# Kernel optimization log

Hardware: AMD Instinct MI355X
Metric: run time of the kernel (lower is better)

The kernel has to match this reference:

```python
import jax, jax.numpy as jnp
import numpy as np

N_ENT = 4096
N_REL = 4
F = 128
BATCH = 8192
ADJ_DENSITY = 0.01


def setup_inputs() -> dict:
    key = jax.random.key(0)
    ks = jax.random.split(key, 8)
    features = jax.random.normal(ks[0], (N_ENT, F), dtype=jnp.float32)
    # sparse binary adjacency per relation (matches count_nonzero degree normalization)
    adj = (jax.random.uniform(ks[1], (N_REL, N_ENT, N_ENT)) < ADJ_DENSITY).astype(jnp.float32)
    W1 = jax.random.normal(ks[2], (N_REL, F, F), dtype=jnp.float32)  # [R, out, in]
    W2 = jax.random.normal(ks[3], (N_REL, F, F), dtype=jnp.float32)
    # DistMult init: diagonal relation matrices (full params, as in the torch code)
    diag_vals = jax.random.normal(ks[4], (N_REL, F), dtype=jnp.float32)
    relmats = jax.vmap(jnp.diag)(diag_vals)  # [R, F, F]
    e1_idx = jax.random.randint(ks[5], (BATCH,), 0, N_ENT)
    rel_idx = jax.random.randint(ks[6], (BATCH,), 0, N_REL)
    e2_idx = jax.random.randint(ks[7], (BATCH,), 0, N_ENT)
    return {"features": features, "adj": adj, "W1": W1, "W2": W2,
            "relmats": relmats, "e1_idx": e1_idx, "rel_idx": rel_idx, "e2_idx": e2_idx}


def _conv_layer(adj, feat, W):
    # degree normalization: 1 / count_nonzero(A_r, dim=1), zeros -> 1
    deg = jnp.sum(adj != 0, axis=2).astype(feat.dtype)            # [R, N]
    inv_deg = 1.0 / jnp.where(deg == 0, 1.0, deg)                 # [R, N]
    agg = jnp.einsum('rnm,mf->rnf', adj, feat)                    # [R, N, F_in]
    y = jnp.einsum('rnf,rof->rno', agg, W)                        # [R, N, F_out] (x @ W_r.T)
    y = jnp.sum(inv_deg[:, :, None] * y, axis=0)                  # [N, F_out]
    return jax.nn.sigmoid(y)


def reference(features, adj, W1, W2, relmats, e1_idx, rel_idx, e2_idx):
    h = _conv_layer(adj, features, W1)
    h = _conv_layer(adj, h, W2)
    # DistMult scores: pred[r] = h @ M_r @ h.T  -> [R, N, N]
    pred = jnp.einsum('nf,rfg,mg->rnm', h, relmats, h)
    # per-sample scalar gather pred[rel][e1][e2]
    return pred[rel_idx, e1_idx, e2_idx]
```

## Files before the change

kernel.cpp:

```cpp
#include <hip/hip_runtime.h>
#include <hip/hip_bf16.h>

#define N_ENT 4096
#define N_REL 4
#define FDIM 128
#define KDIM 512
#define MAXNZ 128
#define BATCH 8192
#define NROWS (N_REL * N_ENT)

typedef float f4v __attribute__((ext_vector_type(4)));

__global__ __launch_bounds__(256) void k_prep(
    const float* __restrict__ W1, const float* __restrict__ W2,
    const float* __restrict__ M, const float* __restrict__ adj,
    const float* __restrict__ feat,
    float* __restrict__ W1T, float* __restrict__ W2T, float* __restrict__ diagM,
    unsigned short* __restrict__ cols, int* __restrict__ cnt,
    float* __restrict__ inv_deg, float* __restrict__ agg) {
  int blk = blockIdx.x;
  if (blk < NROWS) {
    int row = blk;
    int r = row >> 12;
    int node = row & (N_ENT - 1);
    __shared__ unsigned short sc[MAXNZ];
    __shared__ float part[8][FDIM];
    __shared__ int lcnt;
    if (threadIdx.x == 0) lcnt = 0;
    __syncthreads();
    const f4v* src = (const f4v*)(adj + (size_t)row * N_ENT);
    int base = threadIdx.x * 16;
    unsigned mask = 0;
#pragma unroll
    for (int q = 0; q < 4; ++q) {
      f4v v = __builtin_nontemporal_load(src + threadIdx.x * 4 + q);
      if (v.x != 0.f) mask |= 1u << (q * 4 + 0);
      if (v.y != 0.f) mask |= 1u << (q * 4 + 1);
      if (v.z != 0.f) mask |= 1u << (q * 4 + 2);
      if (v.w != 0.f) mask |= 1u << (q * 4 + 3);
    }
    int mycnt = __popc(mask);
    int p = 0;
    if (mycnt) p = atomicAdd(&lcnt, mycnt);
    while (mask) {
      int b = __ffs(mask) - 1;
      mask &= mask - 1;
      if (p < MAXNZ) sc[p] = (unsigned short)(base + b);
      ++p;
    }
    __syncthreads();
    int c = lcnt; if (c > MAXNZ) c = MAXNZ;
    float w = 1.0f / (float)(c > 0 ? c : 1);
    if (threadIdx.x < c) cols[(size_t)row * MAXNZ + threadIdx.x] = sc[threadIdx.x];
    if (threadIdx.x == 0) { cnt[row] = c; inv_deg[row] = w; }
    int l = threadIdx.x & 31;
    int g = threadIdx.x >> 5;
    const float* fp = feat + l * 4;
    float ax = 0.f, ay = 0.f, az = 0.f, aw = 0.f;
    int j = g;
    for (; j + 8 < c; j += 16) {
      float4 v0 = *(const float4*)(fp + (int)sc[j] * FDIM);
      float4 v1 = *(const float4*)(fp + (int)sc[j + 8] * FDIM);
      ax += v0.x + v1.x; ay += v0.y + v1.y;
      az += v0.z + v1.z; aw += v0.w + v1.w;
    }
    if (j < c) {
      float4 v = *(const float4*)(fp + (int)sc[j] * FDIM);
      ax += v.x; ay += v.y; az += v.z; aw += v.w;
    }
    part[g][l * 4 + 0] = ax; part[g][l * 4 + 1] = ay;
    part[g][l * 4 + 2] = az; part[g][l * 4 + 3] = aw;
    __syncthreads();
    if (threadIdx.x < FDIM) {
      float s = 0.f;
#pragma unroll
      for (int gg = 0; gg < 8; ++gg) s += part[gg][threadIdx.x];
      agg[(size_t)node * KDIM + r * FDIM + threadIdx.x] = s * w;
    }
    return;
  }
  int ab = blk - NROWS;
  if (ab < 512) {
    int id = ab * 256 + threadIdx.x;
    int which = id >> 16;
    int e = id & 65535;
    int rr = e >> 14, rem = e & 16383, ff = rem >> 7, o = rem & 127;
    const float* srcw = which ? W2 : W1;
    float* dst = which ? W2T : W1T;
    dst[e] = srcw[(rr * FDIM + o) * FDIM + ff];
    return;
  }
  int idx = (ab - 512) * 256 + threadIdx.x;
  int rr = idx >> 7, ff = idx & 127;
  diagM[idx] = M[((size_t)(rr * FDIM + ff)) * FDIM + ff];
}

__device__ __forceinline__ void gemm_body(
    const float* __restrict__ A, const float* __restrict__ B,
    float* __restrict__ C, int n0, float (*red)[128]) {
  constexpr int KD = KDIM, KH = KDIM / 2, Ncol = FDIM;
  int o = threadIdx.x & 127;
  int half = threadIdx.x >> 7;
  const float* Ap = A + (size_t)n0 * KD + half * KH;
  const float* Bp = B + (size_t)half * KH * Ncol + o;
  float acc[8] = {0.f, 0.f, 0.f, 0.f, 0.f, 0.f, 0.f, 0.f};
#pragma unroll 2
  for (int k = 0; k < KH; k += 4) {
    float4 a0 = *(const float4*)(Ap + 0 * KD + k);
    float4 a1 = *(const float4*)(Ap + 1 * KD + k);
    float4 a2 = *(const float4*)(Ap + 2 * KD + k);
    float4 a3 = *(const float4*)(Ap + 3 * KD + k);
    float4 a4 = *(const float4*)(Ap + 4 * KD + k);
    float4 a5 = *(const float4*)(Ap + 5 * KD + k);
    float4 a6 = *(const float4*)(Ap + 6 * KD + k);
    float4 a7 = *(const float4*)(Ap + 7 * KD + k);
    float b0 = Bp[(size_t)(k + 0) * Ncol];
    float b1 = Bp[(size_t)(k + 1) * Ncol];
    float b2 = Bp[(size_t)(k + 2) * Ncol];
    float b3 = Bp[(size_t)(k + 3) * Ncol];
    acc[0] += a0.x * b0 + a0.y * b1 + a0.z * b2 + a0.w * b3;
    acc[1] += a1.x * b0 + a1.y * b1 + a1.z * b2 + a1.w * b3;
    acc[2] += a2.x * b0 + a2.y * b1 + a2.z * b2 + a2.w * b3;
    acc[3] += a3.x * b0 + a3.y * b1 + a3.z * b2 + a3.w * b3;
    acc[4] += a4.x * b0 + a4.y * b1 + a4.z * b2 + a4.w * b3;
    acc[5] += a5.x * b0 + a5.y * b1 + a5.z * b2 + a5.w * b3;
    acc[6] += a6.x * b0 + a6.y * b1 + a6.z * b2 + a6.w * b3;
    acc[7] += a7.x * b0 + a7.y * b1 + a7.z * b2 + a7.w * b3;
  }
  if (half) {
#pragma unroll
    for (int i = 0; i < 8; ++i) red[i][o] = acc[i];
  }
  __syncthreads();
  if (!half) {
#pragma unroll
    for (int i = 0; i < 8; ++i) {
      float v = acc[i] + red[i][o];
      v = 1.f / (1.f + __expf(-v));
      C[(size_t)(n0 + i) * Ncol + o] = v;
    }
  }
}

__global__ __launch_bounds__(256) void k_gemm(
    const float* __restrict__ A, const float* __restrict__ B,
    float* __restrict__ C) {
  __shared__ float red[8][128];
  gemm_body(A, B, C, blockIdx.x * 8, red);
}

__global__ __launch_bounds__(256) void k_layer2(
    const unsigned short* __restrict__ cols, const int* __restrict__ cnt,
    const float* __restrict__ inv_deg, const float* __restrict__ h1,
    const float* __restrict__ W2T, float* __restrict__ h2) {
  int n0 = blockIdx.x * 4;
  __shared__ unsigned short lc[4][N_REL][MAXNZ];
  __shared__ __align__(16) float aggL[4][KDIM];
  __shared__ float red[4][128];
  {
    int i = threadIdx.x >> 4;
    int t16 = threadIdx.x & 15;
    int nb = i >> 2, r = i & 3;
    int row = r * N_ENT + n0 + nb;
    int c = cnt[row];
    for (int j = t16; j < c; j += 16)
      lc[nb][r][j] = cols[(size_t)row * MAXNZ + j];
  }
  __syncthreads();
  {
    int l = threadIdx.x & 31;
    int g = threadIdx.x >> 5;
    const float* fp = h1 + l * 4;
#pragma unroll
    for (int q = 0; q < 2; ++q) {
      int pair = g + q * 8;
      int nb = pair >> 2, r = pair & 3;
      int row = r * N_ENT + n0 + nb;
      int c = cnt[row];
      float w = inv_deg[row];
      float ax = 0.f, ay = 0.f, az = 0.f, aw = 0.f;
      int j = 0;
      for (; j + 2 <= c; j += 2) {
        float4 v0 = *(const float4*)(fp + (int)lc[nb][r][j] * FDIM);
        float4 v1 = *(const float4*)(fp + (int)lc[nb][r][j + 1] * FDIM);
        ax += v0.x + v1.x; ay += v0.y + v1.y;
        az += v0.z + v1.z; aw += v0.w + v1.w;
      }
      if (j < c) {
        float4 v = *(const float4*)(fp + (int)lc[nb][r][j] * FDIM);
        ax += v.x; ay += v.y; az += v.z; aw += v.w;
      }
      float4 res; res.x = ax * w; res.y = ay * w; res.z = az * w; res.w = aw * w;
      *(float4*)&aggL[nb][r * FDIM + l * 4] = res;
    }
  }
  __syncthreads();
  {
    constexpr int KH = KDIM / 2, Ncol = FDIM;
    int o = threadIdx.x & 127;
    int half = threadIdx.x >> 7;
    const float* Bp = W2T + (size_t)half * KH * Ncol + o;
    int kbase = half * KH;
    float acc[4] = {0.f, 0.f, 0.f, 0.f};
#pragma unroll 2
    for (int k = 0; k < KH; k += 4) {
      float4 a0 = *(const float4*)&aggL[0][kbase + k];
      float4 a1 = *(const float4*)&aggL[1][kbase + k];
      float4 a2 = *(const float4*)&aggL[2][kbase + k];
      float4 a3 = *(const float4*)&aggL[3][kbase + k];
      float b0 = Bp[(size_t)(k + 0) * Ncol];
      float b1 = Bp[(size_t)(k + 1) * Ncol];
      float b2 = Bp[(size_t)(k + 2) * Ncol];
      float b3 = Bp[(size_t)(k + 3) * Ncol];
      acc[0] += a0.x * b0 + a0.y * b1 + a0.z * b2 + a0.w * b3;
      acc[1] += a1.x * b0 + a1.y * b1 + a1.z * b2 + a1.w * b3;
      acc[2] += a2.x * b0 + a2.y * b1 + a2.z * b2 + a2.w * b3;
      acc[3] += a3.x * b0 + a3.y * b1 + a3.z * b2 + a3.w * b3;
    }
    if (half) {
#pragma unroll
      for (int i = 0; i < 4; ++i) red[i][o] = acc[i];
    }
    __syncthreads();
    if (!half) {
#pragma unroll
      for (int i = 0; i < 4; ++i) {
        float v = acc[i] + red[i][o];
        v = 1.f / (1.f + __expf(-v));
        h2[(size_t)(n0 + i) * Ncol + o] = v;
      }
    }
  }
}

__global__ __launch_bounds__(256) void k_score(
    const float* __restrict__ h, const float* __restrict__ diagM,
    const int* __restrict__ e1, const int* __restrict__ rel,
    const int* __restrict__ e2, float* __restrict__ out) {
  int wave = threadIdx.x >> 6;
  int lane = threadIdx.x & 63;
  int b = blockIdx.x * 4 + wave;
  int a = e1[b], r = rel[b], c = e2[b];
  const float* hp = h + (size_t)a * FDIM;
  const float* dp = diagM + (size_t)r * FDIM;
  const float* gp = h + (size_t)c * FDIM;
  float v = hp[lane] * dp[lane] * gp[lane]
          + hp[lane + 64] * dp[lane + 64] * gp[lane + 64];
#pragma unroll
  for (int off = 32; off > 0; off >>= 1) v += __shfl_down(v, off, 64);
  if (lane == 0) out[b] = v;
}

extern "C" void kernel_launch(void* const* d_in, const int* in_sizes, int n_in,
                              void* d_out, int out_size, void* d_ws, size_t ws_size,
                              hipStream_t stream) {
  const float* feat = (const float*)d_in[0];
  const float* adj  = (const float*)d_in[1];
  const float* W1   = (const float*)d_in[2];
  const float* W2   = (const float*)d_in[3];
  const float* M    = (const float*)d_in[4];
  const int* e1     = (const int*)d_in[5];
  const int* rel    = (const int*)d_in[6];
  const int* e2     = (const int*)d_in[7];
  float* out = (float*)d_out;

  char* ws = (char*)d_ws;
  unsigned short* cols = (unsigned short*)(ws);
  int*   cnt  = (int*)  (ws + 4194304);
  float* inv  = (float*)(ws + 4259840);
  float* W1T  = (float*)(ws + 4325376);
  float* W2T  = (float*)(ws + 4587520);
  float* dM   = (float*)(ws + 4849664);
  float* agg  = (float*)(ws + 5111808);
  float* h1   = (float*)(ws + 13500416);
  float* h2   = (float*)(ws + 15597568);

  k_prep<<<NROWS + 514, 256, 0, stream>>>(
      W1, W2, M, adj, feat, W1T, W2T, dM, cols, cnt, inv, agg);

  k_gemm<<<N_ENT / 8, 256, 0, stream>>>(agg, W1T, h1);
  k_layer2<<<N_ENT / 4, 256, 0, stream>>>(cols, cnt, inv, h1, W2T, h2);
  k_score<<<BATCH / 4, 256, 0, stream>>>(h2, dM, e1, rel, e2, out);
}
```

Measured before the change: 463.0 us.

## Fuse all stages into one cooperative persistent kernel with grid syncs

Replaces the four separate launches (prep, layer-1 GEMM, layer-2, scoring) with a single cooperative kernel of 1024 persistent blocks. The blocks loop over each stage's work items and use grid-wide syncs between stages, so three kernel launches and their gaps go away. The cost is less parallelism in the adjacency scan, since 1024 blocks now stride over 16K rows, plus system-scope fences and grid barriers. The layer-1 GEMM also moves from 8 to 4 rows per block. If the cooperative launch fails, it falls back to the old multi-kernel path.

```diff
diff --git a/kernel.cpp b/kernel.cpp
--- a/kernel.cpp
+++ b/kernel.cpp
@@ -1,5 +1,7 @@
 #include <hip/hip_runtime.h>
-#include <hip/hip_bf16.h>
+#include <hip/hip_cooperative_groups.h>
+
+namespace cg = cooperative_groups;
 
 #define N_ENT 4096
 #define N_REL 4
@@ -8,8 +10,258 @@
 #define MAXNZ 128
 #define BATCH 8192
 #define NROWS (N_REL * N_ENT)
+#define GRID 1024
 
 typedef float f4v __attribute__((ext_vector_type(4)));
+
+union SharedU {
+  struct {
+    unsigned short sc[MAXNZ];
+    float part[8][FDIM];
+    int lcnt;
+  } a;
+  struct {
+    unsigned short lc[4][N_REL][MAXNZ];
+    float aggL[4][KDIM];
+    float red[4][FDIM];
+  } c;
+  struct {
+    float red[4][FDIM];
+  } b;
+};
+
+__global__ __launch_bounds__(256, 4) void k_fused(
+    const float* __restrict__ W1, const float* __restrict__ W2,
+    const float* __restrict__ M, const float* __restrict__ adj,
+    const float* __restrict__ feat,
+    const int* __restrict__ e1, const int* __restrict__ rel,
+    const int* __restrict__ e2,
+    float* __restrict__ W1T, float* __restrict__ W2T,
+    float* __restrict__ diagM,
+    unsigned short* __restrict__ cols, int* __restrict__ cnt,
+    float* __restrict__ inv_deg, float* __restrict__ agg,
+    float* __restrict__ h1, float* __restrict__ h2,
+    float* __restrict__ out) {
+  cg::grid_group grid = cg::this_grid();
+  __shared__ __align__(16) union SharedU S;
+  const int tid = threadIdx.x;
+
+  for (int u = blockIdx.x; u < NROWS + 514; u += GRID) {
+    if (u < NROWS) {
+      int row = u;
+      int r = row >> 12;
+      int node = row & (N_ENT - 1);
+      if (tid == 0) S.a.lcnt = 0;
+      __syncthreads();
+      const f4v* src = (const f4v*)(adj + (size_t)row * N_ENT);
+      int base = tid * 16;
+      unsigned mask = 0;
+#pragma unroll
+      for (int q = 0; q < 4; ++q) {
+        f4v v = __builtin_nontemporal_load(src + tid * 4 + q);
+        if (v.x != 0.f) mask |= 1u << (q * 4 + 0);
+        if (v.y != 0.f) mask |= 1u << (q * 4 + 1);
+        if (v.z != 0.f) mask |= 1u << (q * 4 + 2);
+        if (v.w != 0.f) mask |= 1u << (q * 4 + 3);
+      }
+      int mycnt = __popc(mask);
+      int p = 0;
+      if (mycnt) p = atomicAdd(&S.a.lcnt, mycnt);
+      while (mask) {
+        int b = __ffs(mask) - 1;
+        mask &= mask - 1;
+        if (p < MAXNZ) S.a.sc[p] = (unsigned short)(base + b);
+        ++p;
+      }
+      __syncthreads();
+      int c = S.a.lcnt; if (c > MAXNZ) c = MAXNZ;
+      float w = 1.0f / (float)(c > 0 ? c : 1);
+      if (tid < c) cols[(size_t)row * MAXNZ + tid] = S.a.sc[tid];
+      if (tid == 0) { cnt[row] = c; inv_deg[row] = w; }
+      int l = tid & 31;
+      int g = tid >> 5;
+      const float* fp = feat + l * 4;
+      float ax = 0.f, ay = 0.f, az = 0.f, aw = 0.f;
+      int j = g;
+      for (; j + 8 < c; j += 16) {
+        float4 v0 = *(const float4*)(fp + (int)S.a.sc[j] * FDIM);
+        float4 v1 = *(const float4*)(fp + (int)S.a.sc[j + 8] * FDIM);
+        ax += v0.x + v1.x; ay += v0.y + v1.y;
+        az += v0.z + v1.z; aw += v0.w + v1.w;
+      }
+      if (j < c) {
+        float4 v = *(const float4*)(fp + (int)S.a.sc[j] * FDIM);
+        ax += v.x; ay += v.y; az += v.z; aw += v.w;
+      }
+      S.a.part[g][l * 4 + 0] = ax; S.a.part[g][l * 4 + 1] = ay;
+      S.a.part[g][l * 4 + 2] = az; S.a.part[g][l * 4 + 3] = aw;
+      __syncthreads();
+      if (tid < FDIM) {
+        float s = 0.f;
+#pragma unroll
+        for (int gg = 0; gg < 8; ++gg) s += S.a.part[gg][tid];
+        agg[(size_t)node * KDIM + r * FDIM + tid] = s * w;
+      }
+    } else if (u < NROWS + 512) {
+      int ab = u - NROWS;
+      int id = ab * 256 + tid;
+      int which = id >> 16;
+      int e = id & 65535;
+      int rr = e >> 14, rem = e & 16383, ff = rem >> 7, o = rem & 127;
+      const float* srcw = which ? W2 : W1;
+      float* dst = which ? W2T : W1T;
+      dst[e] = srcw[(rr * FDIM + o) * FDIM + ff];
+    } else {
+      int idx = (u - NROWS - 512) * 256 + tid;
+      if (idx < 512) {
+        int rr = idx >> 7, ff = idx & 127;
+        diagM[idx] = M[((size_t)(rr * FDIM + ff)) * FDIM + ff];
+      }
+    }
+  }
+  __threadfence_system();
+  grid.sync();
+  __threadfence_system();
+
+  for (int u = blockIdx.x; u < N_ENT / 4; u += GRID) {
+    constexpr int KH = KDIM / 2, Ncol = FDIM;
+    int o = tid & 127;
+    int half = tid >> 7;
+    int n0 = u * 4;
+    const float* Ap = agg + (size_t)n0 * KDIM + half * KH;
+    const float* Bp = W1T + (size_t)half * KH * Ncol + o;
+    float acc[4] = {0.f, 0.f, 0.f, 0.f};
+#pragma unroll 2
+    for (int k = 0; k < KH; k += 4) {
+      float4 a0 = *(const float4*)(Ap + 0 * KDIM + k);
+      float4 a1 = *(const float4*)(Ap + 1 * KDIM + k);
+      float4 a2 = *(const float4*)(Ap + 2 * KDIM + k);
+      float4 a3 = *(const float4*)(Ap + 3 * KDIM + k);
+      float b0 = Bp[(size_t)(k + 0) * Ncol];
+      float b1 = Bp[(size_t)(k + 1) * Ncol];
+      float b2 = Bp[(size_t)(k + 2) * Ncol];
+      float b3 = Bp[(size_t)(k + 3) * Ncol];
+      acc[0] += a0.x * b0 + a0.y * b1 + a0.z * b2 + a0.w * b3;
+      acc[1] += a1.x * b0 + a1.y * b1 + a1.z * b2 + a1.w * b3;
+      acc[2] += a2.x * b0 + a2.y * b1 + a2.z * b2 + a2.w * b3;
+      acc[3] += a3.x * b0 + a3.y * b1 + a3.z * b2 + a3.w * b3;
+    }
+    if (half) {
+#pragma unroll
+      for (int i = 0; i < 4; ++i) S.b.red[i][o] = acc[i];
+    }
+    __syncthreads();
+    if (!half) {
+#pragma unroll
+      for (int i = 0; i < 4; ++i) {
+        float v = acc[i] + S.b.red[i][o];
+        v = 1.f / (1.f + __expf(-v));
+        h1[(size_t)(n0 + i) * Ncol + o] = v;
+      }
+    }
+    __syncthreads();
+  }
+  __threadfence_system();
+  grid.sync();
+  __threadfence_system();
+
+  for (int u = blockIdx.x; u < N_ENT / 4; u += GRID) {
+    int n0 = u * 4;
+    {
+      int i = tid >> 4;
+      int t16 = tid & 15;
+      int nb = i >> 2, r = i & 3;
+      int row = r * N_ENT + n0 + nb;
+      int c = cnt[row];
+      for (int j = t16; j < c; j += 16)
+        S.c.lc[nb][r][j] = cols[(size_t)row * MAXNZ + j];
+    }
+    __syncthreads();
+    {
+      int l = tid & 31;
+      int g = tid >> 5;
+      const float* fp = h1 + l * 4;
+#pragma unroll
+      for (int q = 0; q < 2; ++q) {
+        int pair = g + q * 8;
+        int nb = pair >> 2, r = pair & 3;
+        int row = r * N_ENT + n0 + nb;
+        int c = cnt[row];
+        float w = inv_deg[row];
+        float ax = 0.f, ay = 0.f, az = 0.f, aw = 0.f;
+        int j = 0;
+        for (; j + 2 <= c; j += 2) {
+          float4 v0 = *(const float4*)(fp + (int)S.c.lc[nb][r][j] * FDIM);
+          float4 v1 = *(const float4*)(fp + (int)S.c.lc[nb][r][j + 1] * FDIM);
+          ax += v0.x + v1.x; ay += v0.y + v1.y;
+          az += v0.z + v1.z; aw += v0.w + v1.w;
+        }
+        if (j < c) {
+          float4 v = *(const float4*)(fp + (int)S.c.lc[nb][r][j] * FDIM);
+          ax += v.x; ay += v.y; az += v.z; aw += v.w;
+        }
+        float4 res; res.x = ax * w; res.y = ay * w; res.z = az * w; res.w = aw * w;
+        *(float4*)&S.c.aggL[nb][r * FDIM + l * 4] = res;
+      }
+    }
+    __syncthreads();
+    {
+      constexpr int KH = KDIM / 2, Ncol = FDIM;
+      int o = tid & 127;
+      int half = tid >> 7;
+      const float* Bp = W2T + (size_t)half * KH * Ncol + o;
+      int kbase = half * KH;
+      float acc[4] = {0.f, 0.f, 0.f, 0.f};
+#pragma unroll 2
+      for (int k = 0; k < KH; k += 4) {
+        float4 a0 = *(const float4*)&S.c.aggL[0][kbase + k];
+        float4 a1 = *(const float4*)&S.c.aggL[1][kbase + k];
+        float4 a2 = *(const float4*)&S.c.aggL[2][kbase + k];
+        float4 a3 = *(const float4*)&S.c.aggL[3][kbase + k];
+        float b0 = Bp[(size_t)(k + 0) * Ncol];
+        float b1 = Bp[(size_t)(k + 1) * Ncol];
+        float b2 = Bp[(size_t)(k + 2) * Ncol];
+        float b3 = Bp[(size_t)(k + 3) * Ncol];
+        acc[0] += a0.x * b0 + a0.y * b1 + a0.z * b2 + a0.w * b3;
+        acc[1] += a1.x * b0 + a1.y * b1 + a1.z * b2 + a1.w * b3;
+        acc[2] += a2.x * b0 + a2.y * b1 + a2.z * b2 + a2.w * b3;
+        acc[3] += a3.x * b0 + a3.y * b1 + a3.z * b2 + a3.w * b3;
+      }
+      if (half) {
+#pragma unroll
+        for (int i = 0; i < 4; ++i) S.c.red[i][o] = acc[i];
+      }
+      __syncthreads();
+      if (!half) {
+#pragma unroll
+        for (int i = 0; i < 4; ++i) {
+          float v = acc[i] + S.c.red[i][o];
+          v = 1.f / (1.f + __expf(-v));
+          h2[(size_t)(n0 + i) * Ncol + o] = v;
+        }
+      }
+    }
+    __syncthreads();
+  }
+  __threadfence_system();
+  grid.sync();
+  __threadfence_system();
+
+  for (int u = blockIdx.x; u < BATCH / 4; u += GRID) {
+    int wave = tid >> 6;
+    int lane = tid & 63;
+    int b = u * 4 + wave;
+    int a_ = e1[b], r_ = rel[b], c_ = e2[b];
+    const float* hp = h2 + (size_t)a_ * FDIM;
+    const float* dp = diagM + (size_t)r_ * FDIM;
+    const float* gp = h2 + (size_t)c_ * FDIM;
+    float v = hp[lane] * dp[lane] * gp[lane]
+            + hp[lane + 64] * dp[lane + 64] * gp[lane + 64];
+#pragma unroll
+    for (int off = 32; off > 0; off >>= 1) v += __shfl_down(v, off, 64);
+    if (lane == 0) out[b] = v;
+  }
+}
 
 __global__ __launch_bounds__(256) void k_prep(
     const float* __restrict__ W1, const float* __restrict__ W2,
@@ -275,10 +527,21 @@
   float* h1   = (float*)(ws + 13500416);
   float* h2   = (float*)(ws + 15597568);
 
-  k_prep<<<NROWS + 514, 256, 0, stream>>>(
-      W1, W2, M, adj, feat, W1T, W2T, dM, cols, cnt, inv, agg);
-
-  k_gemm<<<N_ENT / 8, 256, 0, stream>>>(agg, W1T, h1);
-  k_layer2<<<N_ENT / 4, 256, 0, stream>>>(cols, cnt, inv, h1, W2T, h2);
-  k_score<<<BATCH / 4, 256, 0, stream>>>(h2, dM, e1, rel, e2, out);
-}
+  void* args[] = {
+    (void*)&W1, (void*)&W2, (void*)&M, (void*)&adj, (void*)&feat,
+    (void*)&e1, (void*)&rel, (void*)&e2,
+    (void*)&W1T, (void*)&W2T, (void*)&dM,
+    (void*)&cols, (void*)&cnt, (void*)&inv, (void*)&agg,
+    (void*)&h1, (void*)&h2, (void*)&out
+  };
+  hipError_t err = hipLaunchCooperativeKernel(
+      (const void*)k_fused, dim3(GRID), dim3(256), args, 0, stream);
+  if (err != hipSuccess) {
+    (void)hipGetLastError();
+    k_prep<<<NROWS + 514, 256, 0, stream>>>(
+        W1, W2, M, adj, feat, W1T, W2T, dM, cols, cnt, inv, agg);
+    k_gemm<<<N_ENT / 8, 256, 0, stream>>>(agg, W1T, h1);
+    k_layer2<<<N_ENT / 4, 256, 0, stream>>>(cols, cnt, inv, h1, W2T, h2);
+    k_score<<<BATCH / 4, 256, 0, stream>>>(h2, dM, e1, rel, e2, out);
+  }
+}
```

New measurement: 1.310 ms. 183% more time.
